# Kernel tuning notes

Measured on AMD Instinct MI355X. Metric: run time of the kernel, lower is better.

## Reference

```python
import jax, jax.numpy as jnp
import numpy as np

N_NODES = 50000
N_EDGES = 800000
D = 128


def _degrees(idx, n):
    # in/out degree via segment_sum of ones, clamped to >=1 (DGL clamp)
    ones = jnp.ones(idx.shape[0], dtype=jnp.float32)
    return jnp.clip(jax.ops.segment_sum(ones, idx, num_segments=n), 1.0)


def graph_conv(x, src, dst, W, b):
    # DGL GraphConv, norm='both', aggregate-then-matmul (in_feats == out_feats)
    n = x.shape[0]
    deg_out = _degrees(src, n)  # [N]
    deg_in = _degrees(dst, n)   # [N]
    xs = x * jax.lax.rsqrt(deg_out)[:, None]          # [N, D] pre-normalize
    msg = jax.ops.segment_sum(xs[src], dst, num_segments=n)  # gather+scatter [N, D]
    h = msg * jax.lax.rsqrt(deg_in)[:, None]
    return h @ W + b


def setup_inputs() -> dict:
    key = jax.random.key(0)
    k1, k2, k3, k4, k5 = jax.random.split(key, 5)
    x = jax.random.normal(k1, (N_NODES, D), dtype=jnp.float32)
    src = jax.random.randint(k2, (N_EDGES,), 0, N_NODES, dtype=jnp.int64)
    dst = jax.random.randint(k3, (N_EDGES,), 0, N_NODES, dtype=jnp.int64)
    scale = 1.0 / np.sqrt(D)
    W1 = jax.random.normal(k4, (D, D), dtype=jnp.float32) * scale
    W2 = jax.random.normal(k5, (D, D), dtype=jnp.float32) * scale
    b1 = jnp.zeros((D,), dtype=jnp.float32)
    b2 = jnp.zeros((D,), dtype=jnp.float32)
    return {"x": x, "src": src, "dst": dst, "W1": W1, "b1": b1, "W2": W2, "b2": b2}


def reference(x, src, dst, W1, b1, W2, b2):
    h = graph_conv(x, src, dst, W1, b1)
    h = jax.nn.relu(h)
    return graph_conv(h, src, dst, W2, b2)
```

## Files before the change

### kernel.cpp

```cpp
#include <hip/hip_runtime.h>

#define N_NODES 50000
#define N_EDGES 800000
#define D 128
#define CAP 48
#define OVF_CAP 4096

#define BINS 40
#define PNODES 1250
#define B1 64
#define CH1 ((N_EDGES + B1 - 1) / B1)
#define NW (N_NODES / 4)
#define WPB ((NW + B1 - 1) / B1)

typedef unsigned short bf16_t;
typedef __attribute__((ext_vector_type(8))) short short8v;
typedef __attribute__((ext_vector_type(4))) float f32x4;

__device__ inline float bf2f(bf16_t u) {
    union { unsigned int i; float f; } v;
    v.i = ((unsigned int)u) << 16;
    return v.f;
}
__device__ inline bf16_t f2bf(float f) {
    union { float f; unsigned int i; } v;
    v.f = f;
    unsigned int u = v.i;
    unsigned int r = (u + 0x7FFFu + ((u >> 16) & 1u)) >> 16;
    return (bf16_t)r;
}
__device__ inline float u2f_lo(unsigned int u) {
    union { unsigned int i; float f; } x; x.i = u << 16; return x.f;
}
__device__ inline float u2f_hi(unsigned int u) {
    union { unsigned int i; float f; } x; x.i = u & 0xFFFF0000u; return x.f;
}

__global__ __launch_bounds__(1024) void hist40_kernel(const int* __restrict__ src,
                                                      const int* __restrict__ dst,
                                                      unsigned int* __restrict__ H40,
                                                      unsigned int* __restrict__ SH,
                                                      int* __restrict__ ovf_cnt, int nE) {
    __shared__ unsigned int hb[BINS];
    __shared__ unsigned int hs[NW];
    if (blockIdx.x == 0 && threadIdx.x == 0) ovf_cnt[0] = 0;
    for (int i = threadIdx.x; i < NW; i += 1024) hs[i] = 0u;
    if (threadIdx.x < BINS) hb[threadIdx.x] = 0u;
    __syncthreads();
    int e0 = blockIdx.x * CH1;
    int e1 = min(e0 + CH1, nE);
    for (int e = e0 + (int)threadIdx.x; e < e1; e += 1024) {
        int s = src[e];
        int d = dst[e];
        atomicAdd(&hs[s >> 2], 1u << (8 * (s & 3)));
        atomicAdd(&hb[d / PNODES], 1u);
    }
    __syncthreads();
    if (threadIdx.x < BINS) H40[blockIdx.x * BINS + threadIdx.x] = hb[threadIdx.x];
    unsigned int* SHb = SH + (size_t)blockIdx.x * NW;
    for (int i = threadIdx.x; i < NW; i += 1024) SHb[i] = hs[i];
}

__global__ void scan40_kernel(const unsigned int* __restrict__ H40,
                              unsigned int* __restrict__ OFF40,
                              unsigned int* __restrict__ binBase,
                              unsigned int* __restrict__ binTot) {
    __shared__ unsigned int part[B1 * BINS];
    __shared__ unsigned int tot[BINS], base[BINS];
    int j = (int)threadIdx.x;
    if (j < BINS) {
        unsigned int run = 0;
        for (int b = 0; b < B1; b++) {
            part[b * BINS + j] = run;
            run += H40[b * BINS + j];
        }
        tot[j] = run;
    }
    __syncthreads();
    if (j == 0) {
        unsigned int run = 0;
        for (int q = 0; q < BINS; q++) { base[q] = run; run += tot[q]; }
    }
    __syncthreads();
    if (j < BINS) {
        binBase[j] = base[j];
        binTot[j] = tot[j];
        for (int b = 0; b < B1; b++) OFF40[b * BINS + j] = part[b * BINS + j] + base[j];
    }
}

__global__ __launch_bounds__(1024) void place40_kernel(const int* __restrict__ src,
                                                       const int* __restrict__ dst,
                                                       const unsigned int* __restrict__ OFF40,
                                                       unsigned int* __restrict__ binned,
                                                       const unsigned int* __restrict__ SH,
                                                       int* __restrict__ cnt_s, int nE) {
    __shared__ unsigned int cur[BINS];
    if (threadIdx.x < BINS) cur[threadIdx.x] = OFF40[blockIdx.x * BINS + threadIdx.x];
    __syncthreads();
    int e0 = blockIdx.x * CH1;
    int e1 = min(e0 + CH1, nE);
    for (int e = e0 + (int)threadIdx.x; e < e1; e += 1024) {
        int s = src[e];
        int d = dst[e];
        int bin = d / PNODES;
        unsigned int pos = atomicAdd(&cur[bin], 1u);
        binned[pos] = (unsigned int)(d - bin * PNODES) | ((unsigned int)s << 16);
    }
    int w = blockIdx.x * WPB + (int)threadIdx.x;
    if ((int)threadIdx.x < WPB && w < NW) {
        unsigned int run = 0;
#pragma unroll 8
        for (int b = 0; b < B1; b++) run += SH[(size_t)b * NW + w];
        int4 c;
        c.x = (int)(run & 0xFFu); c.y = (int)((run >> 8) & 0xFFu);
        c.z = (int)((run >> 16) & 0xFFu); c.w = (int)(run >> 24);
        ((int4*)cnt_s)[w] = c;
    }
}

__global__ __launch_bounds__(1024) void scatter2_kernel(
    const unsigned int* __restrict__ binned, const unsigned int* __restrict__ binBase,
    const unsigned int* __restrict__ binTot, unsigned short* __restrict__ bucket,
    int* __restrict__ cnt_d, int* __restrict__ ovf_cnt, int2* __restrict__ ovf) {
    __shared__ unsigned short bk[PNODES * CAP];
    __shared__ unsigned int cur[PNODES];
    const int j = blockIdx.x;
    const int nbeg = j * PNODES;
    for (int i = threadIdx.x; i < PNODES; i += 1024) cur[i] = 0u;
    __syncthreads();
    unsigned int b0 = binBase[j];
    unsigned int n = binTot[j];
    for (unsigned int i = threadIdx.x; i < n; i += 1024) {
        unsigned int v = binned[b0 + i];
        unsigned int dl = v & 0xFFFFu;
        unsigned int s = v >> 16;
        unsigned int q = atomicAdd(&cur[dl], 1u);
        if (q < CAP) {
            bk[dl * CAP + q] = (unsigned short)s;
        } else {
            int o = atomicAdd(ovf_cnt, 1);
            if (o < OVF_CAP) ovf[o] = make_int2(nbeg + (int)dl, (int)s);
        }
    }
    __syncthreads();
    uint4* gb = (uint4*)(bucket + (size_t)nbeg * CAP);
    const uint4* lb = (const uint4*)bk;
    const int n16 = PNODES * CAP * 2 / 16;
    for (int i = threadIdx.x; i < n16; i += 1024) gb[i] = lb[i];
    for (int i = threadIdx.x; i < PNODES; i += 1024) cnt_d[nbeg + i] = (int)cur[i];
}

__global__ void prescale_kernel(const float4* __restrict__ x, const int* __restrict__ cnt_s,
                                const int* __restrict__ cnt_d,
                                float* __restrict__ rs_out, float* __restrict__ rs_in,
                                ushort4* __restrict__ xs4, int nN) {
    int node = blockIdx.x * 8 + (threadIdx.x >> 5);
    int c = threadIdx.x & 31;
    if (node >= nN) return;
    float rs_o = 0.0f;
    if (c == 0) {
        rs_o = rsqrtf(fmaxf((float)cnt_s[node], 1.0f));
        rs_out[node] = rs_o;
        rs_in[node] = rsqrtf(fmaxf((float)cnt_d[node], 1.0f));
    }
    rs_o = __shfl(rs_o, threadIdx.x & 32);
    float4 v = x[(size_t)node * 32 + c];
    ushort4 o;
    o.x = f2bf(v.x * rs_o);
    o.y = f2bf(v.y * rs_o);
    o.z = f2bf(v.z * rs_o);
    o.w = f2bf(v.w * rs_o);
    xs4[(size_t)node * 32 + c] = o;
}

__global__ void wsplit_kernel(const float* __restrict__ W1, bf16_t* __restrict__ Wf1,
                              const float* __restrict__ W2, bf16_t* __restrict__ Wf2) {
    const float* W = blockIdx.y ? W2 : W1;
    bf16_t* Wf = blockIdx.y ? Wf2 : Wf1;
    int flat = blockIdx.x * 256 + (int)threadIdx.x;
    int lane = flat & 63;
    int c = (flat >> 6) & 7;
    int ks = flat >> 9;
    int n = c * 16 + (lane & 15);
    int kb = ks * 32 + (lane >> 4) * 8;
#pragma unroll
    for (int j = 0; j < 8; j++) {
        float w = W[(size_t)(kb + j) * D + n];
        bf16_t hi = f2bf(w);
        bf16_t lo = f2bf(w - bf2f(hi));
        Wf[(size_t)flat * 8 + j] = hi;
        Wf[(size_t)(2048 + flat) * 8 + j] = lo;
    }
}

#define LDW 132
template <bool RELU_OUTSCALE, bool OUT_BF16>
__global__ __launch_bounds__(512) void fused_layer_kernel(
    const uint4* __restrict__ xsrc,
    const int* __restrict__ cnt_d,
    const unsigned short* __restrict__ bucket,
    const int* __restrict__ ovf_cnt, const int2* __restrict__ ovf,
    const float* __restrict__ rs_in, const float* __restrict__ rs_out,
    const bf16_t* __restrict__ Wf, const float* __restrict__ bias,
    void* __restrict__ outp, int nN) {
    __shared__ float sA[64 * LDW];
    int tid = (int)threadIdx.x;
    int n0 = blockIdx.x * 64;
    int lane16 = tid & 15;
    int grp = tid >> 4;

#define ACC8(v)                                              \
    a[0] += u2f_lo(v.x); a[1] += u2f_hi(v.x);                \
    a[2] += u2f_lo(v.y); a[3] += u2f_hi(v.y);                \
    a[4] += u2f_lo(v.z); a[5] += u2f_hi(v.z);                \
    a[6] += u2f_lo(v.w); a[7] += u2f_hi(v.w);
#pragma unroll
    for (int r = 0; r < 2; r++) {
        int ln = r * 32 + grp;
        int node = n0 + ln;
        float a[8];
#pragma unroll
        for (int k = 0; k < 8; k++) a[k] = 0.f;
        if (node < nN) {
            const unsigned short* bk = bucket + (size_t)node * CAP;
            int cnt = min(cnt_d[node], CAP);
            int e = 0;
            for (; e + 3 < cnt; e += 4) {
                int s0 = bk[e], s1 = bk[e + 1], s2 = bk[e + 2], s3 = bk[e + 3];
                uint4 v0 = xsrc[(size_t)s0 * 16 + lane16];
                uint4 v1 = xsrc[(size_t)s1 * 16 + lane16];
                uint4 v2 = xsrc[(size_t)s2 * 16 + lane16];
                uint4 v3 = xsrc[(size_t)s3 * 16 + lane16];
                ACC8(v0) ACC8(v1) ACC8(v2) ACC8(v3)
            }
            for (; e < cnt; e++) {
                int s0 = bk[e];
                uint4 v0 = xsrc[(size_t)s0 * 16 + lane16];
                ACC8(v0)
            }
        }
        float* row = sA + ln * LDW + lane16 * 8;
#pragma unroll
        for (int k = 0; k < 8; k++) row[k] = a[k];
    }
#undef ACC8

    int novf = min(*ovf_cnt, OVF_CAP);
    if (novf > 0) {
        __syncthreads();
        for (int i = tid; i < novf; i += 512) {
            int2 ds = ovf[i];
            int ln = ds.x - n0;
            if ((unsigned)ln < 64u) {
                const uint4* xr = xsrc + (size_t)ds.y * 16;
                for (int c = 0; c < 16; c++) {
                    uint4 v = xr[c];
                    float* q = sA + ln * LDW + c * 8;
                    atomicAdd(q + 0, u2f_lo(v.x)); atomicAdd(q + 1, u2f_hi(v.x));
                    atomicAdd(q + 2, u2f_lo(v.y)); atomicAdd(q + 3, u2f_hi(v.y));
                    atomicAdd(q + 4, u2f_lo(v.z)); atomicAdd(q + 5, u2f_hi(v.z));
                    atomicAdd(q + 6, u2f_lo(v.w)); atomicAdd(q + 7, u2f_hi(v.w));
                }
            }
        }
    }
    __syncthreads();

    int lane = tid & 63;
    int wave = tid >> 6;
    int tile = wave >> 1;
    int half = wave & 1;
    int ar = lane & 15;
    int kg = lane >> 4;
    const float* ap = sA + (tile * 16 + ar) * LDW + kg * 8;
    short8v ahi[4], alo[4];
#pragma unroll
    for (int ks = 0; ks < 4; ks++) {
#pragma unroll
        for (int j = 0; j < 8; j++) {
            float av = ap[ks * 32 + j];
            bf16_t h = f2bf(av);
            ahi[ks][j] = (short)h;
            alo[ks][j] = (short)f2bf(av - bf2f(h));
        }
    }

    f32x4 acc[4];
#pragma unroll
    for (int c = 0; c < 4; c++) acc[c] = (f32x4){0.f, 0.f, 0.f, 0.f};

    const short8v* Bh = (const short8v*)Wf;
    const short8v* Bl = Bh + 2048;
#pragma unroll
    for (int ks = 0; ks < 4; ks++) {
#pragma unroll
        for (int c = 0; c < 4; c++) {
            int off = (ks * 8 + half * 4 + c) * 64 + lane;
            short8v wh = Bh[off];
            short8v wl = Bl[off];
            acc[c] = __builtin_amdgcn_mfma_f32_16x16x32_bf16(ahi[ks], wh, acc[c], 0, 0, 0);
            acc[c] = __builtin_amdgcn_mfma_f32_16x16x32_bf16(alo[ks], wh, acc[c], 0, 0, 0);
            acc[c] = __builtin_amdgcn_mfma_f32_16x16x32_bf16(ahi[ks], wl, acc[c], 0, 0, 0);
        }
    }

    int ocol = lane & 15;
#pragma unroll
    for (int r = 0; r < 4; r++) {
        int node = n0 + tile * 16 + kg * 4 + r;
        if (node >= nN) continue;
        float ri = rs_in[node];
        float ro = RELU_OUTSCALE ? rs_out[node] : 1.0f;
#pragma unroll
        for (int c = 0; c < 4; c++) {
            int col = half * 64 + c * 16 + ocol;
            float v = acc[c][r] * ri + bias[col];
            if (RELU_OUTSCALE) v = fmaxf(v, 0.0f) * ro;
            if (OUT_BF16) {
                ((bf16_t*)outp)[(size_t)node * D + col] = f2bf(v);
            } else {
                ((float*)outp)[(size_t)node * D + col] = v;
            }
        }
    }
}
#undef LDW

static inline size_t align16(size_t x) { return (x + 15) & ~(size_t)15; }

extern "C" void kernel_launch(void* const* d_in, const int* in_sizes, int n_in,
                              void* d_out, int out_size, void* d_ws, size_t ws_size,
                              hipStream_t stream) {
    const float* x   = (const float*)d_in[0];
    const int*   src = (const int*)d_in[1];
    const int*   dst = (const int*)d_in[2];
    const float* W1  = (const float*)d_in[3];
    const float* b1  = (const float*)d_in[4];
    const float* W2  = (const float*)d_in[5];
    const float* b2  = (const float*)d_in[6];
    float* out = (float*)d_out;

    char* p = (char*)d_ws;
    int*            cnt_s   = (int*)p;            p += align16(N_NODES * sizeof(int));
    int*            cnt_d   = (int*)p;            p += align16(N_NODES * sizeof(int));
    int*            ovf_cnt = (int*)p;            p += align16(16 * sizeof(int));
    int2*           ovf     = (int2*)p;           p += align16((size_t)OVF_CAP * sizeof(int2));
    unsigned short* bucket  = (unsigned short*)p; p += align16((size_t)N_NODES * CAP * sizeof(unsigned short));
    float*          rs_out  = (float*)p;          p += align16(N_NODES * sizeof(float));
    float*          rs_in   = (float*)p;          p += align16(N_NODES * sizeof(float));
    bf16_t*         Wf1     = (bf16_t*)p;         p += align16((size_t)2 * 2048 * 8 * sizeof(bf16_t));
    bf16_t*         Wf2     = (bf16_t*)p;         p += align16((size_t)2 * 2048 * 8 * sizeof(bf16_t));
    unsigned int*   H40     = (unsigned int*)p;   p += align16((size_t)B1 * BINS * sizeof(unsigned int));
    unsigned int*   OFF40   = (unsigned int*)p;   p += align16((size_t)B1 * BINS * sizeof(unsigned int));
    unsigned int*   binBase = (unsigned int*)p;   p += align16(BINS * sizeof(unsigned int));
    unsigned int*   binTot  = (unsigned int*)p;   p += align16(BINS * sizeof(unsigned int));
    unsigned int*   binned  = (unsigned int*)p;   p += align16((size_t)N_EDGES * sizeof(unsigned int));
    unsigned int*   SH      = (unsigned int*)p;   p += align16((size_t)B1 * NW * sizeof(unsigned int));
    bf16_t*         xs      = (bf16_t*)p;         p += align16((size_t)N_NODES * D * sizeof(bf16_t));
    bf16_t*         hs      = (bf16_t*)p;

    wsplit_kernel<<<dim3(8, 2), 256, 0, stream>>>(W1, Wf1, W2, Wf2);

    hist40_kernel<<<B1, 1024, 0, stream>>>(src, dst, H40, SH, ovf_cnt, N_EDGES);
    scan40_kernel<<<1, 64, 0, stream>>>(H40, OFF40, binBase, binTot);
    place40_kernel<<<B1, 1024, 0, stream>>>(src, dst, OFF40, binned, SH, cnt_s, N_EDGES);
    scatter2_kernel<<<BINS, 1024, 0, stream>>>(binned, binBase, binTot, bucket,
                                               cnt_d, ovf_cnt, ovf);

    prescale_kernel<<<(N_NODES + 7) / 8, 256, 0, stream>>>((const float4*)x, cnt_s, cnt_d,
                                                           rs_out, rs_in, (ushort4*)xs, N_NODES);

    int fgrid = (N_NODES + 63) / 64;

    fused_layer_kernel<true, true><<<fgrid, 512, 0, stream>>>(
        (const uint4*)xs, cnt_d, bucket, ovf_cnt, ovf, rs_in, rs_out, Wf1, b1, hs, N_NODES);

    fused_layer_kernel<false, false><<<fgrid, 512, 0, stream>>>(
        (const uint4*)hs, cnt_d, bucket, ovf_cnt, ovf, rs_in, rs_out, Wf2, b2, out, N_NODES);
}
```

Before: 197.1 us.

## Widen histogram grid, parallelize scan, split scatter bins, rework fused layer blocking

The edge-binning pipeline now uses 256 histogram blocks instead of 64. The scan becomes a per-bin parallel prefix over blocks, and bin bases are recomputed inside the place and scatter kernels instead of stored. The scatter stage splits each bin into two half-blocks, which doubles the grid and halves shared memory per block. The fused layer now handles 32 nodes per 1024-thread block: it stages bucket indices in shared memory, uses 32 lanes per node with 8-byte gathers, and has each wave compute one 16-column MFMA job. SH aliases the hs buffer to save workspace. This relies on hs not being written until after place40 has consumed SH.

Result: slower. 248.1 us (+25.9%).

```diff
diff --git a/kernel.cpp b/kernel.cpp
--- a/kernel.cpp
+++ b/kernel.cpp
@@ -8,7 +8,8 @@
 
 #define BINS 40
 #define PNODES 1250
-#define B1 64
+#define SN 625
+#define B1 256
 #define CH1 ((N_EDGES + B1 - 1) / B1)
 #define NW (N_NODES / 4)
 #define WPB ((NW + B1 - 1) / B1)
@@ -61,54 +62,55 @@
     for (int i = threadIdx.x; i < NW; i += 1024) SHb[i] = hs[i];
 }
 
-__global__ void scan40_kernel(const unsigned int* __restrict__ H40,
-                              unsigned int* __restrict__ OFF40,
-                              unsigned int* __restrict__ binBase,
-                              unsigned int* __restrict__ binTot) {
-    __shared__ unsigned int part[B1 * BINS];
-    __shared__ unsigned int tot[BINS], base[BINS];
-    int j = (int)threadIdx.x;
-    if (j < BINS) {
-        unsigned int run = 0;
-        for (int b = 0; b < B1; b++) {
-            part[b * BINS + j] = run;
-            run += H40[b * BINS + j];
-        }
-        tot[j] = run;
-    }
-    __syncthreads();
-    if (j == 0) {
-        unsigned int run = 0;
-        for (int q = 0; q < BINS; q++) { base[q] = run; run += tot[q]; }
-    }
-    __syncthreads();
-    if (j < BINS) {
-        binBase[j] = base[j];
-        binTot[j] = tot[j];
-        for (int b = 0; b < B1; b++) OFF40[b * BINS + j] = part[b * BINS + j] + base[j];
-    }
+__global__ __launch_bounds__(B1) void scan40_kernel(const unsigned int* __restrict__ H40,
+                                                    unsigned int* __restrict__ OFF40,
+                                                    unsigned int* __restrict__ binTot) {
+    __shared__ unsigned int sc[B1];
+    int j = (int)blockIdx.x;
+    int t = (int)threadIdx.x;
+    unsigned int own = H40[t * BINS + j];
+    sc[t] = own;
+    __syncthreads();
+    for (int off = 1; off < B1; off <<= 1) {
+        unsigned int v = (t >= off) ? sc[t - off] : 0u;
+        __syncthreads();
+        sc[t] += v;
+        __syncthreads();
+    }
+    OFF40[t * BINS + j] = sc[t] - own;
+    if (t == B1 - 1) binTot[j] = sc[t];
 }
 
 __global__ __launch_bounds__(1024) void place40_kernel(const int* __restrict__ src,
                                                        const int* __restrict__ dst,
                                                        const unsigned int* __restrict__ OFF40,
+                                                       const unsigned int* __restrict__ binTot,
                                                        unsigned int* __restrict__ binned,
                                                        const unsigned int* __restrict__ SH,
                                                        int* __restrict__ cnt_s, int nE) {
     __shared__ unsigned int cur[BINS];
-    if (threadIdx.x < BINS) cur[threadIdx.x] = OFF40[blockIdx.x * BINS + threadIdx.x];
+    __shared__ unsigned int bb[BINS];
+    int t = (int)threadIdx.x;
+    if (t < BINS) bb[t] = binTot[t];
+    __syncthreads();
+    if (t == 0) {
+        unsigned int r = 0;
+        for (int q = 0; q < BINS; q++) { unsigned int v = bb[q]; bb[q] = r; r += v; }
+    }
+    __syncthreads();
+    if (t < BINS) cur[t] = OFF40[blockIdx.x * BINS + t] + bb[t];
     __syncthreads();
     int e0 = blockIdx.x * CH1;
     int e1 = min(e0 + CH1, nE);
-    for (int e = e0 + (int)threadIdx.x; e < e1; e += 1024) {
+    for (int e = e0 + t; e < e1; e += 1024) {
         int s = src[e];
         int d = dst[e];
         int bin = d / PNODES;
         unsigned int pos = atomicAdd(&cur[bin], 1u);
         binned[pos] = (unsigned int)(d - bin * PNODES) | ((unsigned int)s << 16);
     }
-    int w = blockIdx.x * WPB + (int)threadIdx.x;
-    if ((int)threadIdx.x < WPB && w < NW) {
+    int w = blockIdx.x * WPB + t;
+    if (t < WPB && w < NW) {
         unsigned int run = 0;
 #pragma unroll 8
         for (int b = 0; b < B1; b++) run += SH[(size_t)b * NW + w];
@@ -120,35 +122,48 @@
 }
 
 __global__ __launch_bounds__(1024) void scatter2_kernel(
-    const unsigned int* __restrict__ binned, const unsigned int* __restrict__ binBase,
-    const unsigned int* __restrict__ binTot, unsigned short* __restrict__ bucket,
-    int* __restrict__ cnt_d, int* __restrict__ ovf_cnt, int2* __restrict__ ovf) {
-    __shared__ unsigned short bk[PNODES * CAP];
-    __shared__ unsigned int cur[PNODES];
-    const int j = blockIdx.x;
-    const int nbeg = j * PNODES;
-    for (int i = threadIdx.x; i < PNODES; i += 1024) cur[i] = 0u;
-    __syncthreads();
-    unsigned int b0 = binBase[j];
+    const unsigned int* __restrict__ binned, const unsigned int* __restrict__ binTot,
+    unsigned short* __restrict__ bucket, int* __restrict__ cnt_d,
+    int* __restrict__ ovf_cnt, int2* __restrict__ ovf) {
+    __shared__ unsigned short bk[SN * CAP];
+    __shared__ unsigned int cur[SN];
+    __shared__ unsigned int bb[BINS];
+    int t = (int)threadIdx.x;
+    int j = (int)blockIdx.x >> 1;
+    int h = (int)blockIdx.x & 1;
+    if (t < BINS) bb[t] = binTot[t];
+    __syncthreads();
+    if (t == 0) {
+        unsigned int r = 0;
+        for (int q = 0; q < BINS; q++) { unsigned int v = bb[q]; bb[q] = r; r += v; }
+    }
+    for (int i = t; i < SN; i += 1024) cur[i] = 0u;
+    __syncthreads();
+    unsigned int b0 = bb[j];
     unsigned int n = binTot[j];
-    for (unsigned int i = threadIdx.x; i < n; i += 1024) {
+    int lo = h * SN;
+    int nbeg = j * PNODES + lo;
+    for (unsigned int i = t; i < n; i += 1024) {
         unsigned int v = binned[b0 + i];
-        unsigned int dl = v & 0xFFFFu;
-        unsigned int s = v >> 16;
-        unsigned int q = atomicAdd(&cur[dl], 1u);
-        if (q < CAP) {
-            bk[dl * CAP + q] = (unsigned short)s;
-        } else {
-            int o = atomicAdd(ovf_cnt, 1);
-            if (o < OVF_CAP) ovf[o] = make_int2(nbeg + (int)dl, (int)s);
+        int dl = (int)(v & 0xFFFFu);
+        int dl2 = dl - lo;
+        if ((unsigned)dl2 < (unsigned)SN) {
+            unsigned int s = v >> 16;
+            unsigned int q = atomicAdd(&cur[dl2], 1u);
+            if (q < CAP) {
+                bk[dl2 * CAP + q] = (unsigned short)s;
+            } else {
+                int o = atomicAdd(ovf_cnt, 1);
+                if (o < OVF_CAP) ovf[o] = make_int2(j * PNODES + dl, (int)s);
+            }
         }
     }
     __syncthreads();
     uint4* gb = (uint4*)(bucket + (size_t)nbeg * CAP);
     const uint4* lb = (const uint4*)bk;
-    const int n16 = PNODES * CAP * 2 / 16;
-    for (int i = threadIdx.x; i < n16; i += 1024) gb[i] = lb[i];
-    for (int i = threadIdx.x; i < PNODES; i += 1024) cnt_d[nbeg + i] = (int)cur[i];
+    const int n16 = SN * CAP * 2 / 16;
+    for (int i = t; i < n16; i += 1024) gb[i] = lb[i];
+    for (int i = t; i < SN; i += 1024) cnt_d[nbeg + i] = (int)cur[i];
 }
 
 __global__ void prescale_kernel(const float4* __restrict__ x, const int* __restrict__ cnt_s,
@@ -196,71 +211,72 @@
 
 #define LDW 132
 template <bool RELU_OUTSCALE, bool OUT_BF16>
-__global__ __launch_bounds__(512) void fused_layer_kernel(
-    const uint4* __restrict__ xsrc,
+__global__ __launch_bounds__(1024, 8) void fused_layer_kernel(
+    const uint2* __restrict__ xs2,
     const int* __restrict__ cnt_d,
     const unsigned short* __restrict__ bucket,
     const int* __restrict__ ovf_cnt, const int2* __restrict__ ovf,
     const float* __restrict__ rs_in, const float* __restrict__ rs_out,
     const bf16_t* __restrict__ Wf, const float* __restrict__ bias,
     void* __restrict__ outp, int nN) {
-    __shared__ float sA[64 * LDW];
+    __shared__ float sA[32 * LDW];
+    __shared__ unsigned short sb[32 * CAP];
     int tid = (int)threadIdx.x;
-    int n0 = blockIdx.x * 64;
-    int lane16 = tid & 15;
-    int grp = tid >> 4;
-
-#define ACC8(v)                                              \
-    a[0] += u2f_lo(v.x); a[1] += u2f_hi(v.x);                \
-    a[2] += u2f_lo(v.y); a[3] += u2f_hi(v.y);                \
-    a[4] += u2f_lo(v.z); a[5] += u2f_hi(v.z);                \
-    a[6] += u2f_lo(v.w); a[7] += u2f_hi(v.w);
-#pragma unroll
-    for (int r = 0; r < 2; r++) {
-        int ln = r * 32 + grp;
+    int n0 = blockIdx.x * 32;
+
+    if (tid < 32 * 6) {
+        int ln = tid / 6, w = tid % 6;
         int node = n0 + ln;
-        float a[8];
-#pragma unroll
-        for (int k = 0; k < 8; k++) a[k] = 0.f;
-        if (node < nN) {
-            const unsigned short* bk = bucket + (size_t)node * CAP;
-            int cnt = min(cnt_d[node], CAP);
-            int e = 0;
-            for (; e + 3 < cnt; e += 4) {
-                int s0 = bk[e], s1 = bk[e + 1], s2 = bk[e + 2], s3 = bk[e + 3];
-                uint4 v0 = xsrc[(size_t)s0 * 16 + lane16];
-                uint4 v1 = xsrc[(size_t)s1 * 16 + lane16];
-                uint4 v2 = xsrc[(size_t)s2 * 16 + lane16];
-                uint4 v3 = xsrc[(size_t)s3 * 16 + lane16];
-                ACC8(v0) ACC8(v1) ACC8(v2) ACC8(v3)
-            }
-            for (; e < cnt; e++) {
-                int s0 = bk[e];
-                uint4 v0 = xsrc[(size_t)s0 * 16 + lane16];
-                ACC8(v0)
-            }
-        }
-        float* row = sA + ln * LDW + lane16 * 8;
-#pragma unroll
-        for (int k = 0; k < 8; k++) row[k] = a[k];
-    }
-#undef ACC8
+        uint4 v = make_uint4(0u, 0u, 0u, 0u);
+        if (node < nN) v = ((const uint4*)(bucket + (size_t)node * CAP))[w];
+        ((uint4*)sb)[ln * 6 + w] = v;
+    }
+    __syncthreads();
+
+    int row = tid >> 5;
+    int lane32 = tid & 31;
+    int node = n0 + row;
+    float a0 = 0.f, a1 = 0.f, a2 = 0.f, a3 = 0.f;
+#define ACC4(v)                                  \
+    a0 += u2f_lo(v.x); a1 += u2f_hi(v.x);        \
+    a2 += u2f_lo(v.y); a3 += u2f_hi(v.y);
+    if (node < nN) {
+        const unsigned short* bkl = sb + row * CAP;
+        int cnt = min(cnt_d[node], CAP);
+        int e = 0;
+        for (; e + 3 < cnt; e += 4) {
+            int s0 = bkl[e], s1 = bkl[e + 1], s2 = bkl[e + 2], s3 = bkl[e + 3];
+            uint2 v0 = xs2[(size_t)s0 * 32 + lane32];
+            uint2 v1 = xs2[(size_t)s1 * 32 + lane32];
+            uint2 v2 = xs2[(size_t)s2 * 32 + lane32];
+            uint2 v3 = xs2[(size_t)s3 * 32 + lane32];
+            ACC4(v0) ACC4(v1) ACC4(v2) ACC4(v3)
+        }
+        for (; e < cnt; e++) {
+            int s0 = bkl[e];
+            uint2 v0 = xs2[(size_t)s0 * 32 + lane32];
+            ACC4(v0)
+        }
+    }
+#undef ACC4
+    {
+        float* rp = sA + row * LDW + lane32 * 4;
+        rp[0] = a0; rp[1] = a1; rp[2] = a2; rp[3] = a3;
+    }
 
     int novf = min(*ovf_cnt, OVF_CAP);
     if (novf > 0) {
         __syncthreads();
-        for (int i = tid; i < novf; i += 512) {
+        for (int i = tid; i < novf; i += 1024) {
             int2 ds = ovf[i];
             int ln = ds.x - n0;
-            if ((unsigned)ln < 64u) {
-                const uint4* xr = xsrc + (size_t)ds.y * 16;
-                for (int c = 0; c < 16; c++) {
-                    uint4 v = xr[c];
-                    float* q = sA + ln * LDW + c * 8;
+            if ((unsigned)ln < 32u) {
+                const uint2* xr = xs2 + (size_t)ds.y * 32;
+                for (int c = 0; c < 32; c++) {
+                    uint2 v = xr[c];
+                    float* q = sA + ln * LDW + c * 4;
                     atomicAdd(q + 0, u2f_lo(v.x)); atomicAdd(q + 1, u2f_hi(v.x));
                     atomicAdd(q + 2, u2f_lo(v.y)); atomicAdd(q + 3, u2f_hi(v.y));
-                    atomicAdd(q + 4, u2f_lo(v.z)); atomicAdd(q + 5, u2f_hi(v.z));
-                    atomicAdd(q + 6, u2f_lo(v.w)); atomicAdd(q + 7, u2f_hi(v.w));
                 }
             }
         }
@@ -269,59 +285,52 @@
 
     int lane = tid & 63;
     int wave = tid >> 6;
-    int tile = wave >> 1;
-    int half = wave & 1;
+    int tile = wave >> 3;
+    int job = wave & 7;
     int ar = lane & 15;
     int kg = lane >> 4;
     const float* ap = sA + (tile * 16 + ar) * LDW + kg * 8;
     short8v ahi[4], alo[4];
 #pragma unroll
     for (int ks = 0; ks < 4; ks++) {
+        float4 p0 = *(const float4*)(ap + ks * 32);
+        float4 p1 = *(const float4*)(ap + ks * 32 + 4);
+        float av[8] = {p0.x, p0.y, p0.z, p0.w, p1.x, p1.y, p1.z, p1.w};
 #pragma unroll
         for (int j = 0; j < 8; j++) {
-            float av = ap[ks * 32 + j];
-            bf16_t h = f2bf(av);
-            ahi[ks][j] = (short)h;
-            alo[ks][j] = (short)f2bf(av - bf2f(h));
-        }
-    }
-
-    f32x4 acc[4];
-#pragma unroll
-    for (int c = 0; c < 4; c++) acc[c] = (f32x4){0.f, 0.f, 0.f, 0.f};
-
+            bf16_t hh = f2bf(av[j]);
+            ahi[ks][j] = (short)hh;
+            alo[ks][j] = (short)f2bf(av[j] - bf2f(hh));
+        }
+    }
+
+    f32x4 acc = (f32x4){0.f, 0.f, 0.f, 0.f};
     const short8v* Bh = (const short8v*)Wf;
     const short8v* Bl = Bh + 2048;
 #pragma unroll
     for (int ks = 0; ks < 4; ks++) {
-#pragma unroll
-        for (int c = 0; c < 4; c++) {
-            int off = (ks * 8 + half * 4 + c) * 64 + lane;
-            short8v wh = Bh[off];
-            short8v wl = Bl[off];
-            acc[c] = __builtin_amdgcn_mfma_f32_16x16x32_bf16(ahi[ks], wh, acc[c], 0, 0, 0);
-            acc[c] = __builtin_amdgcn_mfma_f32_16x16x32_bf16(alo[ks], wh, acc[c], 0, 0, 0);
-            acc[c] = __builtin_amdgcn_mfma_f32_16x16x32_bf16(ahi[ks], wl, acc[c], 0, 0, 0);
-        }
+        int off = (ks * 8 + job) * 64 + lane;
+        short8v wh = Bh[off];
+        short8v wl = Bl[off];
+        acc = __builtin_amdgcn_mfma_f32_16x16x32_bf16(ahi[ks], wh, acc, 0, 0, 0);
+        acc = __builtin_amdgcn_mfma_f32_16x16x32_bf16(alo[ks], wh, acc, 0, 0, 0);
+        acc = __builtin_amdgcn_mfma_f32_16x16x32_bf16(ahi[ks], wl, acc, 0, 0, 0);
     }
 
     int ocol = lane & 15;
+    int col = job * 16 + ocol;
+    float bv = bias[col];
 #pragma unroll
     for (int r = 0; r < 4; r++) {
-        int node = n0 + tile * 16 + kg * 4 + r;
-        if (node >= nN) continue;
-        float ri = rs_in[node];
-        float ro = RELU_OUTSCALE ? rs_out[node] : 1.0f;
-#pragma unroll
-        for (int c = 0; c < 4; c++) {
-            int col = half * 64 + c * 16 + ocol;
-            float v = acc[c][r] * ri + bias[col];
-            if (RELU_OUTSCALE) v = fmaxf(v, 0.0f) * ro;
-            if (OUT_BF16) {
-                ((bf16_t*)outp)[(size_t)node * D + col] = f2bf(v);
-            } else {
-                ((float*)outp)[(size_t)node * D + col] = v;
-            }
+        int onode = n0 + tile * 16 + kg * 4 + r;
+        if (onode >= nN) continue;
+        float ri = rs_in[onode];
+        float v = acc[r] * ri + bv;
+        if (RELU_OUTSCALE) v = fmaxf(v, 0.0f) * rs_out[onode];
+        if (OUT_BF16) {
+            ((bf16_t*)outp)[(size_t)onode * D + col] = f2bf(v);
+        } else {
+            ((float*)outp)[(size_t)onode * D + col] = v;
         }
     }
 }
@@ -353,29 +362,27 @@
     bf16_t*         Wf2     = (bf16_t*)p;         p += align16((size_t)2 * 2048 * 8 * sizeof(bf16_t));
     unsigned int*   H40     = (unsigned int*)p;   p += align16((size_t)B1 * BINS * sizeof(unsigned int));
     unsigned int*   OFF40   = (unsigned int*)p;   p += align16((size_t)B1 * BINS * sizeof(unsigned int));
-    unsigned int*   binBase = (unsigned int*)p;   p += align16(BINS * sizeof(unsigned int));
     unsigned int*   binTot  = (unsigned int*)p;   p += align16(BINS * sizeof(unsigned int));
     unsigned int*   binned  = (unsigned int*)p;   p += align16((size_t)N_EDGES * sizeof(unsigned int));
-    unsigned int*   SH      = (unsigned int*)p;   p += align16((size_t)B1 * NW * sizeof(unsigned int));
     bf16_t*         xs      = (bf16_t*)p;         p += align16((size_t)N_NODES * D * sizeof(bf16_t));
     bf16_t*         hs      = (bf16_t*)p;
+    unsigned int*   SH      = (unsigned int*)hs;
 
     wsplit_kernel<<<dim3(8, 2), 256, 0, stream>>>(W1, Wf1, W2, Wf2);
 
     hist40_kernel<<<B1, 1024, 0, stream>>>(src, dst, H40, SH, ovf_cnt, N_EDGES);
-    scan40_kernel<<<1, 64, 0, stream>>>(H40, OFF40, binBase, binTot);
-    place40_kernel<<<B1, 1024, 0, stream>>>(src, dst, OFF40, binned, SH, cnt_s, N_EDGES);
-    scatter2_kernel<<<BINS, 1024, 0, stream>>>(binned, binBase, binTot, bucket,
-                                               cnt_d, ovf_cnt, ovf);
+    scan40_kernel<<<BINS, B1, 0, stream>>>(H40, OFF40, binTot);
+    place40_kernel<<<B1, 1024, 0, stream>>>(src, dst, OFF40, binTot, binned, SH, cnt_s, N_EDGES);
+    scatter2_kernel<<<BINS * 2, 1024, 0, stream>>>(binned, binTot, bucket, cnt_d, ovf_cnt, ovf);
 
     prescale_kernel<<<(N_NODES + 7) / 8, 256, 0, stream>>>((const float4*)x, cnt_s, cnt_d,
                                                            rs_out, rs_in, (ushort4*)xs, N_NODES);
 
-    int fgrid = (N_NODES + 63) / 64;
-
-    fused_layer_kernel<true, true><<<fgrid, 512, 0, stream>>>(
-        (const uint4*)xs, cnt_d, bucket, ovf_cnt, ovf, rs_in, rs_out, Wf1, b1, hs, N_NODES);
-
-    fused_layer_kernel<false, false><<<fgrid, 512, 0, stream>>>(
-        (const uint4*)hs, cnt_d, bucket, ovf_cnt, ovf, rs_in, rs_out, Wf2, b2, out, N_NODES);
-}
+    int fgrid = (N_NODES + 31) / 32;
+
+    fused_layer_kernel<true, true><<<fgrid, 1024, 0, stream>>>(
+        (const uint2*)xs, cnt_d, bucket, ovf_cnt, ovf, rs_in, rs_out, Wf1, b1, hs, N_NODES);
+
+    fused_layer_kernel<false, false><<<fgrid, 1024, 0, stream>>>(
+        (const uint2*)hs, cnt_d, bucket, ovf_cnt, ovf, rs_in, rs_out, Wf2, b2, out, N_NODES);
+}
```
